# Kernel optimization log

Hardware: AMD Instinct MI355X
Metric: run time of the kernel (lower is better)

The kernel has to match this reference:

```python
import jax, jax.numpy as jnp
import numpy as np

N, E = 10000, 100000   # nodes, edges
C = 64                 # sphere_channels
L2 = 9                 # (lmax+1)^2 with lmax=2
H, DH, DV = 8, 16, 16  # heads, alpha channels/head, value channels/head
EC = 64                # edge scalar channels
NRBF = 128             # radial basis size
ZMAX = 90              # max_num_elements


def setup_inputs() -> dict:
    key = jax.random.key(0)
    ks = jax.random.split(key, 12)
    inp = {}
    inp["node_embedding"] = jax.random.normal(ks[0], (N, L2, C), jnp.float32)
    inp["atomic_numbers"] = jax.random.randint(ks[1], (N,), 0, ZMAX)
    inp["edge_distance"] = jax.random.uniform(ks[2], (E,), jnp.float32)
    inp["edge_index"] = jax.random.randint(ks[3], (2, E), 0, N)
    # per-edge Wigner rotation into the edge-aligned SO(2) frame
    inp["wigner"] = jax.random.normal(ks[4], (E, L2, L2), jnp.float32) / np.sqrt(L2)
    # learned parameters
    inp["atom_emb"] = jax.random.normal(ks[5], (ZMAX, EC), jnp.float32) * 0.1
    inp["W_rbf"] = jax.random.normal(ks[6], (NRBF, EC), jnp.float32) / np.sqrt(NRBF)
    inp["W_gate"] = jax.random.normal(ks[7], (EC, H * DH), jnp.float32) / np.sqrt(EC)
    inp["W_msg"] = jax.random.normal(ks[8], (2 * C, H * DH), jnp.float32) / np.sqrt(2 * C)
    inp["alpha_vec"] = jax.random.normal(ks[9], (H, DH), jnp.float32) / np.sqrt(DH)
    inp["W_val"] = jax.random.normal(ks[10], (H * DH, H * DV), jnp.float32) / np.sqrt(H * DH)
    inp["W_out"] = jax.random.normal(ks[11], (H * DV, 1), jnp.float32) / np.sqrt(H * DV)
    return inp


def reference(node_embedding, atomic_numbers, edge_distance, edge_index, wigner,
              atom_emb, W_rbf, W_gate, W_msg, alpha_vec, W_val, W_out):
    src, dst = edge_index[0], edge_index[1]
    # --- edge scalar embedding: gaussian RBF of distance + endpoint atom embeddings ---
    centers = jnp.linspace(0.0, 1.0, NRBF, dtype=node_embedding.dtype)
    width = 1.0 / NRBF
    rbf = jnp.exp(-((edge_distance[:, None] - centers) ** 2) / (2.0 * width * width))  # [E, NRBF]
    edge_scalar = jax.nn.silu(rbf @ W_rbf + atom_emb[atomic_numbers[src]] + atom_emb[atomic_numbers[dst]])  # [E, EC]
    gate = jax.nn.silu(edge_scalar @ W_gate)  # [E, H*DH]
    # --- gather endpoint embeddings and rotate into edge frame (SO3 rotation) ---
    x_s = jnp.einsum('eij,ejc->eic', wigner, node_embedding[src])  # [E, L2, C]
    x_t = jnp.einsum('eij,ejc->eic', wigner, node_embedding[dst])  # [E, L2, C]
    msg = jnp.concatenate([x_s, x_t], axis=-1) @ W_msg            # [E, L2, H*DH]
    msg = msg * gate[:, None, :]
    # --- attention logits from the invariant (l=0) component ---
    a = msg[:, 0, :].reshape(E, H, DH)
    logits = jnp.einsum('ehd,hd->eh', jax.nn.leaky_relu(a, 0.2), alpha_vec)  # [E, H]
    # --- softmax over incoming edges of each destination node ---
    m = jax.ops.segment_max(logits, dst, num_segments=N)  # [N, H]
    ex = jnp.exp(logits - m[dst])
    den = jax.ops.segment_sum(ex, dst, num_segments=N)
    attn = ex / (den[dst] + 1e-9)  # [E, H]
    # --- attention-weighted values, rotate back, scatter-sum to nodes ---
    v = (msg @ W_val).reshape(E, L2, H, DV)
    v = v * attn[:, None, :, None]
    v = jnp.einsum('eji,ejhv->eihv', wigner, v).reshape(E, L2, H * DV)  # rotate back (R^T)
    node_out = jax.ops.segment_sum(v, dst, num_segments=N)  # [N, L2, H*DV]
    out = node_out @ W_out                                   # [N, L2, 1]
    forces = out[:, 1:4, 0]                                  # narrow(1,1,3).view(-1,3)
    return forces
```

## Files before the change

kernel.cpp:

```cpp
#include <hip/hip_runtime.h>
#include <hip/hip_bf16.h>

#define NN 10000
#define NE 100000

typedef __attribute__((ext_vector_type(8))) short short8v;
typedef __attribute__((ext_vector_type(4))) short short4v;
typedef __attribute__((ext_vector_type(4))) float float4v;

__device__ __forceinline__ unsigned int enc_f(float f) {
  unsigned int u = __float_as_uint(f);
  return (u & 0x80000000u) ? ~u : (u | 0x80000000u);
}
__device__ __forceinline__ float dec_f(unsigned int u) {
  return __uint_as_float((u & 0x80000000u) ? (u & 0x7fffffffu) : ~u);
}
__device__ __forceinline__ float silu_f(float x) {
  return x / (1.0f + __expf(-x));
}
__device__ __forceinline__ float b2f(short s) {
  return __uint_as_float(((unsigned int)(unsigned short)s) << 16);
}
__device__ __forceinline__ void f32_hilo(float x, short& h, short& l) {
  __hip_bfloat16 bh = __float2bfloat16(x);
  float r = x - __bfloat162float(bh);
  __hip_bfloat16 bl = __float2bfloat16(r);
  h = __builtin_bit_cast(short, bh);
  l = __builtin_bit_cast(short, bl);
}
__device__ __forceinline__ short f2bf(float x) {
  return __builtin_bit_cast(short, __float2bfloat16(x));
}
#define MFMA16(a, b, c) __builtin_amdgcn_mfma_f32_16x16x32_bf16(a, b, c, 0, 0, 0)

__global__ void prep_kernel(const float* __restrict__ W_msg, const float* __restrict__ W_val,
                            const float* __restrict__ W_out, const float* __restrict__ W_rbf,
                            const float* __restrict__ W_gate,
                            float* __restrict__ Q,
                            short* __restrict__ Wp1h, short* __restrict__ Wp1l,
                            short* __restrict__ Wp2h, short* __restrict__ Wp2l,
                            short* __restrict__ Wp3h, short* __restrict__ Wp3l,
                            short* __restrict__ Wp4h, short* __restrict__ Wp4l) {
  int i = blockIdx.x * blockDim.x + threadIdx.x;
  if (i < 1024) {
    int c = i >> 3, h = i & 7;
    float s = 0.0f;
#pragma unroll
    for (int dv = 0; dv < 16; ++dv)
      s += W_val[c * 128 + h * 16 + dv] * W_out[h * 16 + dv];
    Q[c * 8 + h] = s;
  }
  const float* W; short* ph; short* pl; int KF, Nw, local; bool tr = false;
  if (i < 8192)       { W = W_rbf;  ph = Wp1h; pl = Wp1l; KF = 4; Nw = 64;  local = i; }
  else if (i < 16384) { W = W_gate; ph = Wp2h; pl = Wp2l; KF = 2; Nw = 128; local = i - 8192; }
  else if (i < 32768) { W = W_msg;  ph = Wp3h; pl = Wp3l; KF = 4; Nw = 128; local = i - 16384; }
  else                { W = W_msg;  ph = Wp4h; pl = Wp4l; KF = 4; Nw = 128; local = i - 32768; tr = true; }
  int tile = local >> 9;
  int ln = (local >> 3) & 63;
  int j = local & 7;
  int nt = tile / KF, kf = tile % KF;
  int k = kf * 32 + 8 * (ln >> 4) + j;
  int n = nt * 16 + (ln & 15);
  float w = tr ? W[n * 128 + k] : W[k * Nw + n];
  short h, lo;
  f32_hilo(w, h, lo);
  ph[local] = h;
  pl[local] = lo;
}

__global__ __launch_bounds__(256) void gather1_kernel(
    const float* __restrict__ nb, const int* __restrict__ ei,
    const float* __restrict__ wig, short* __restrict__ xch,
    short* __restrict__ xcl, short* __restrict__ Gb) {
  const int lane = threadIdx.x & 63;
  const int e = blockIdx.x * 4 + (threadIdx.x >> 6);
  int se = ei[e], de = ei[NE + e];
  const float* __restrict__ pw = wig + (size_t)e * 81;
  const float* __restrict__ ps = nb + (size_t)se * 576 + lane;
  const float* __restrict__ pt = nb + (size_t)de * 576 + lane;
  float vs[9], vt[9];
#pragma unroll
  for (int j = 0; j < 9; ++j) {
    vs[j] = ps[j * 64];
    vt[j] = pt[j * 64];
  }
  float Gs0 = 0, Gs1 = 0, Gs2 = 0, Gt0 = 0, Gt1 = 0, Gt2 = 0;
#pragma unroll
  for (int j = 0; j < 9; ++j) {
    float row[9];
#pragma unroll
    for (int jp = 0; jp < 9; ++jp) row[jp] = pw[j * 9 + jp];
    float xs = 0.0f, xt = 0.0f;
#pragma unroll
    for (int jp = 0; jp < 9; ++jp) { xs += row[jp] * vs[jp]; xt += row[jp] * vt[jp]; }
    if (j == 0) {
      short h, l;
      f32_hilo(xs, h, l);
      xch[(size_t)e * 128 + lane] = h;
      xcl[(size_t)e * 128 + lane] = l;
      f32_hilo(xt, h, l);
      xch[(size_t)e * 128 + 64 + lane] = h;
      xcl[(size_t)e * 128 + 64 + lane] = l;
    }
    Gs0 += row[1] * xs; Gs1 += row[2] * xs; Gs2 += row[3] * xs;
    Gt0 += row[1] * xt; Gt1 += row[2] * xt; Gt2 += row[3] * xt;
  }
  short* gp = Gb + (size_t)e * 384 + lane;
  gp[0]       = f2bf(Gs0);
  gp[64]      = f2bf(Gs1);
  gp[128]     = f2bf(Gs2);
  gp[192]     = f2bf(Gt0);
  gp[256]     = f2bf(Gt1);
  gp[320]     = f2bf(Gt2);
}

__global__ __launch_bounds__(256, 3) void pass1_kernel(
    const int* __restrict__ zn, const float* __restrict__ dist,
    const int* __restrict__ ei, const float* __restrict__ aemb,
    const float* __restrict__ alpha,
    const short* __restrict__ xch, const short* __restrict__ xcl,
    const short* __restrict__ Wp1h, const short* __restrict__ Wp1l,
    const short* __restrict__ Wp2h, const short* __restrict__ Wp2l,
    const short* __restrict__ Wp3h, const short* __restrict__ Wp3l,
    float* __restrict__ logits, unsigned int* __restrict__ m_enc,
    __hip_bfloat16* __restrict__ gate_ws) {
  __shared__ __attribute__((aligned(16))) float es_s[4][16][68];
  const int tid = threadIdx.x;
  const int lane = tid & 63;
  const int wid = tid >> 6;
  const int g = lane >> 4;
  const int col = lane & 15;
  const int e0 = (blockIdx.x * 4 + wid) * 16;

  int l16 = lane & 15;
  int ecl16 = (e0 + l16 < NE) ? e0 + l16 : NE - 1;
  int idx_v = 0;
  if (lane < 32) idx_v = ei[(lane < 16 ? 0 : NE) + ecl16];

  int ecol = e0 + col; if (ecol >= NE) ecol = NE - 1;
  const float d = dist[ecol];

  const short* ph = xch + (size_t)ecol * 128 + 8 * g;
  const short* pl = xcl + (size_t)ecol * 128 + 8 * g;
  short8v a3h[4], a3l[4];
#pragma unroll
  for (int kf = 0; kf < 4; ++kf) {
    a3h[kf] = *(const short8v*)(ph + kf * 32);
    a3l[kf] = *(const short8v*)(pl + kf * 32);
  }

  short8v a1h[4], a1l[4];
#pragma unroll
  for (int kf = 0; kf < 4; ++kf) {
#pragma unroll
    for (int j = 0; j < 8; ++j) {
      int k = kf * 32 + 8 * g + j;
      float t = d - (float)k * (1.0f / 127.0f);
      float v = __expf(-8192.0f * t * t);
      short h, lo; f32_hilo(v, h, lo);
      a1h[kf][j] = h; a1l[kf][j] = lo;
    }
  }

  const float4v z4 = {0.0f, 0.0f, 0.0f, 0.0f};

  float4v acc1[4];
#pragma unroll
  for (int nt = 0; nt < 4; ++nt) {
    float4v a = z4;
#pragma unroll
    for (int kf = 0; kf < 4; ++kf) {
      short8v bh = *(const short8v*)(Wp1h + ((nt * 4 + kf) * 64 + lane) * 8);
      short8v bl = *(const short8v*)(Wp1l + ((nt * 4 + kf) * 64 + lane) * 8);
      a = MFMA16(a1h[kf], bh, a);
      a = MFMA16(a1h[kf], bl, a);
      a = MFMA16(a1l[kf], bh, a);
    }
    acc1[nt] = a;
  }

  int dn_r[4];
#pragma unroll
  for (int r = 0; r < 4; ++r) {
    int sn = __shfl(idx_v, 4 * g + r);
    dn_r[r] = __shfl(idx_v, 16 + 4 * g + r);
    int zs = zn[sn], zd = zn[dn_r[r]];
#pragma unroll
    for (int nt = 0; nt < 4; ++nt) {
      float b = aemb[zs * 64 + nt * 16 + col] + aemb[zd * 64 + nt * 16 + col];
      es_s[wid][4 * g + r][nt * 16 + col] = silu_f(acc1[nt][r] + b);
    }
  }

  short8v a2h[2], a2l[2];
#pragma unroll
  for (int kf = 0; kf < 2; ++kf) {
    const float* p = &es_s[wid][col][kf * 32 + 8 * g];
    float4v v0 = *(const float4v*)p;
    float4v v1 = *(const float4v*)(p + 4);
#pragma unroll
    for (int j = 0; j < 4; ++j) {
      short h, lo;
      f32_hilo(v0[j], h, lo); a2h[kf][j] = h;     a2l[kf][j] = lo;
      f32_hilo(v1[j], h, lo); a2h[kf][4 + j] = h; a2l[kf][4 + j] = lo;
    }
  }

  float gate_r[8][4];
#pragma unroll
  for (int nt = 0; nt < 8; ++nt) {
    float4v a = z4;
#pragma unroll
    for (int kf = 0; kf < 2; ++kf) {
      short8v bh = *(const short8v*)(Wp2h + ((nt * 2 + kf) * 64 + lane) * 8);
      short8v bl = *(const short8v*)(Wp2l + ((nt * 2 + kf) * 64 + lane) * 8);
      a = MFMA16(a2h[kf], bh, a);
      a = MFMA16(a2h[kf], bl, a);
      a = MFMA16(a2l[kf], bh, a);
    }
#pragma unroll
    for (int r = 0; r < 4; ++r) {
      float gv = silu_f(a[r]);
      gate_r[nt][r] = gv;
      int er = e0 + 4 * g + r;
      if (er < NE)
        gate_ws[(size_t)er * 128 + nt * 16 + col] = __float2bfloat16(gv);
    }
  }

#pragma unroll
  for (int nt = 0; nt < 8; ++nt) {
    float4v a = z4;
#pragma unroll
    for (int kf = 0; kf < 4; ++kf) {
      short8v bh = *(const short8v*)(Wp3h + ((nt * 4 + kf) * 64 + lane) * 8);
      short8v bl = *(const short8v*)(Wp3l + ((nt * 4 + kf) * 64 + lane) * 8);
      a = MFMA16(a3h[kf], bh, a);
      a = MFMA16(a3h[kf], bl, a);
      a = MFMA16(a3l[kf], bh, a);
    }
    float al = alpha[nt * 16 + col];
#pragma unroll
    for (int r = 0; r < 4; ++r) {
      float v = a[r] * gate_r[nt][r];
      v = v > 0.0f ? v : 0.2f * v;
      v *= al;
#pragma unroll
      for (int off = 1; off < 16; off <<= 1) v += __shfl_xor(v, off);
      int er = e0 + 4 * g + r;
      if (col == 0 && er < NE) {
        logits[(size_t)er * 8 + nt] = v;
        atomicMax(&m_enc[dn_r[r] * 8 + nt], enc_f(v));
      }
    }
  }
}

__global__ void pass2_kernel(const float* __restrict__ logits,
                             const int* __restrict__ ei,
                             const unsigned int* __restrict__ m_enc,
                             float* __restrict__ den) {
  int i = blockIdx.x * blockDim.x + threadIdx.x;
  if (i >= NE * 8) return;
  int e = i >> 3, h = i & 7;
  int dn = ei[NE + e];
  float mm = dec_f(m_enc[dn * 8 + h]);
  atomicAdd(&den[dn * 8 + h], __expf(logits[i] - mm));
}

__global__ __launch_bounds__(256, 3) void pass3_kernel(
    const int* __restrict__ ei, const float* __restrict__ logits,
    const unsigned int* __restrict__ m_enc, const float* __restrict__ den,
    const __hip_bfloat16* __restrict__ gate_ws, const float* __restrict__ Q,
    const short* __restrict__ Wp4h, const short* __restrict__ Wp4l,
    const short* __restrict__ Gb, float* __restrict__ out) {
  __shared__ __attribute__((aligned(16))) float attn_s[4][16][8];
  __shared__ __attribute__((aligned(16))) float x_s[4][16][132];
  const int tid = threadIdx.x;
  const int lane = tid & 63;
  const int wid = tid >> 6;
  const int g = lane >> 4;
  const int col = lane & 15;
  const int e0 = (blockIdx.x * 4 + wid) * 16;

#pragma unroll
  for (int half = 0; half < 2; ++half) {
    int i = half * 64 + lane;
    int e = i >> 3, h = i & 7;
    int ec = e0 + e; if (ec >= NE) ec = NE - 1;
    int dn = ei[NE + ec];
    float l = logits[(size_t)ec * 8 + h];
    float mm = dec_f(m_enc[dn * 8 + h]);
    float dv = den[dn * 8 + h];
    attn_s[wid][e][h] = __expf(l - mm) / (dv + 1e-9f);
  }

  float q0[8], q1[8];
#pragma unroll
  for (int h = 0; h < 8; ++h) {
    q0[h] = Q[(2 * lane) * 8 + h];
    q1[h] = Q[(2 * lane + 1) * 8 + h];
  }
#pragma unroll 4
  for (int e = 0; e < 16; ++e) {
    int ec = e0 + e; if (ec >= NE) ec = NE - 1;
    float4v a0 = *(const float4v*)&attn_s[wid][e][0];
    float4v a1 = *(const float4v*)&attn_s[wid][e][4];
    float wv0 = 0.0f, wv1 = 0.0f;
#pragma unroll
    for (int h = 0; h < 4; ++h) {
      wv0 += q0[h] * a0[h] + q0[4 + h] * a1[h];
      wv1 += q1[h] * a0[h] + q1[4 + h] * a1[h];
    }
    unsigned int gp = *(const unsigned int*)(gate_ws + (size_t)ec * 128 + 2 * lane);
    float gg0 = __uint_as_float((gp & 0xffffu) << 16);
    float gg1 = __uint_as_float((gp & 0xffff0000u));
    float2 uu; uu.x = gg0 * wv0; uu.y = gg1 * wv1;
    *(float2*)&x_s[wid][e][2 * lane] = uu;
  }

  short8v ah[4], al[4];
#pragma unroll
  for (int kf = 0; kf < 4; ++kf) {
    const float* p = &x_s[wid][col][kf * 32 + 8 * g];
    float4v v0 = *(const float4v*)p;
    float4v v1 = *(const float4v*)(p + 4);
#pragma unroll
    for (int j = 0; j < 4; ++j) {
      short h, lo;
      f32_hilo(v0[j], h, lo); ah[kf][j] = h;     al[kf][j] = lo;
      f32_hilo(v1[j], h, lo); ah[kf][4 + j] = h; al[kf][4 + j] = lo;
    }
  }
  const float4v z4 = {0.0f, 0.0f, 0.0f, 0.0f};
#pragma unroll
  for (int nt = 0; nt < 8; ++nt) {
    float4v a = z4;
#pragma unroll
    for (int kf = 0; kf < 4; ++kf) {
      short8v bh = *(const short8v*)(Wp4h + ((nt * 4 + kf) * 64 + lane) * 8);
      short8v bl = *(const short8v*)(Wp4l + ((nt * 4 + kf) * 64 + lane) * 8);
      a = MFMA16(ah[kf], bh, a);
      a = MFMA16(ah[kf], bl, a);
      a = MFMA16(al[kf], bh, a);
    }
#pragma unroll
    for (int r = 0; r < 4; ++r)
      x_s[wid][4 * g + r][nt * 16 + col] = a[r];
  }

  const int cg = col * 4;
#pragma unroll
  for (int it = 0; it < 4; ++it) {
    int e = it * 4 + g;
    int eu = e0 + e;
    bool valid = eu < NE;
    int ec = valid ? eu : NE - 1;
    int de = ei[NE + ec];
    float4v t0 = *(const float4v*)&x_s[wid][e][cg];
    float4v t1 = *(const float4v*)&x_s[wid][e][64 + cg];
    const short* gp = Gb + (size_t)ec * 384 + cg;
    float p[3];
#pragma unroll
    for (int i = 0; i < 3; ++i) {
      short4v gs = *(const short4v*)(gp + i * 64);
      short4v gt = *(const short4v*)(gp + (3 + i) * 64);
      p[i] = b2f(gs[0]) * t0[0] + b2f(gs[1]) * t0[1] + b2f(gs[2]) * t0[2] + b2f(gs[3]) * t0[3] +
             b2f(gt[0]) * t1[0] + b2f(gt[1]) * t1[1] + b2f(gt[2]) * t1[2] + b2f(gt[3]) * t1[3];
    }
#pragma unroll
    for (int i = 0; i < 3; ++i)
#pragma unroll
      for (int off = 1; off < 16; off <<= 1) p[i] += __shfl_xor(p[i], off);
    float pv = (col == 1) ? p[0] : ((col == 2) ? p[1] : p[2]);
    if (valid && col >= 1 && col <= 3)
      atomicAdd(&out[de * 3 + (col - 1)], pv);
  }
}

extern "C" void kernel_launch(void* const* d_in, const int* in_sizes, int n_in,
                              void* d_out, int out_size, void* d_ws, size_t ws_size,
                              hipStream_t stream) {
  const float* nb = (const float*)d_in[0];
  const int* zn = (const int*)d_in[1];
  const float* dist = (const float*)d_in[2];
  const int* ei = (const int*)d_in[3];
  const float* wig = (const float*)d_in[4];
  const float* aemb = (const float*)d_in[5];
  const float* W_rbf = (const float*)d_in[6];
  const float* W_gate = (const float*)d_in[7];
  const float* W_msg = (const float*)d_in[8];
  const float* alpha = (const float*)d_in[9];
  const float* W_val = (const float*)d_in[10];
  const float* W_out = (const float*)d_in[11];
  float* out = (float*)d_out;

  char* p = (char*)d_ws;
  float* Q = (float*)p;                   p += 1024 * 4;
  unsigned int* m_enc = (unsigned int*)p; p += (size_t)NN * 8 * 4;
  float* den = (float*)p;                 p += (size_t)NN * 8 * 4;
  float* logits = (float*)p;              p += (size_t)NE * 8 * 4;
  __hip_bfloat16* gate_ws = (__hip_bfloat16*)p; p += (size_t)NE * 128 * 2;
  short* Wp1h = (short*)p; p += 8192 * 2;
  short* Wp1l = (short*)p; p += 8192 * 2;
  short* Wp2h = (short*)p; p += 8192 * 2;
  short* Wp2l = (short*)p; p += 8192 * 2;
  short* Wp3h = (short*)p; p += 16384 * 2;
  short* Wp3l = (short*)p; p += 16384 * 2;
  short* Wp4h = (short*)p; p += 16384 * 2;
  short* Wp4l = (short*)p; p += 16384 * 2;
  short* xch = (short*)p;                 p += (size_t)NE * 128 * 2;
  short* xcl = (short*)p;                 p += (size_t)NE * 128 * 2;
  short* Gb = (short*)p;                  p += (size_t)NE * 384 * 2;

  hipMemsetAsync(d_out, 0, (size_t)NN * 3 * 4, stream);
  hipMemsetAsync(m_enc, 0, (size_t)NN * 8 * 4, stream);
  hipMemsetAsync(den, 0, (size_t)NN * 8 * 4, stream);

  prep_kernel<<<192, 256, 0, stream>>>(W_msg, W_val, W_out, W_rbf, W_gate, Q,
                                       Wp1h, Wp1l, Wp2h, Wp2l, Wp3h, Wp3l, Wp4h, Wp4l);
  gather1_kernel<<<NE / 4, 256, 0, stream>>>(nb, ei, wig, xch, xcl, Gb);
  pass1_kernel<<<(NE + 63) / 64, 256, 0, stream>>>(zn, dist, ei, aemb, alpha,
                                                   xch, xcl,
                                                   Wp1h, Wp1l, Wp2h, Wp2l, Wp3h, Wp3l,
                                                   logits, m_enc, gate_ws);
  pass2_kernel<<<(NE * 8 + 255) / 256, 256, 0, stream>>>(logits, ei, m_enc, den);
  pass3_kernel<<<(NE + 63) / 64, 256, 0, stream>>>(ei, logits, m_enc, den,
                                                   gate_ws, Q, Wp4h, Wp4l, Gb, out);
}
```

Measured before the change: 315.3 us.

## Fuse gather/rotation kernel into pass1 with software-pipelined node loads

Removes the separate gather1 kernel and performs the Wigner rotation of source/target node embeddings inside pass1, keeping the l=0 rotated features in shared memory instead of writing hi/lo bf16 copies to global memory and reading them back. Node embedding loads are double-buffered across edges so the next edge's gathers are in flight while the current one is rotated. This cuts a kernel launch and about 51 MB of intermediate traffic, but each wave now processes 16 edges serially in the gather phase, which adds register pressure under launch_bounds(256,3) and may lower parallelism compared with the one-edge-per-wave gather.

```diff
diff --git a/kernel.cpp b/kernel.cpp
--- a/kernel.cpp
+++ b/kernel.cpp
@@ -8,6 +8,9 @@
 typedef __attribute__((ext_vector_type(4))) short short4v;
 typedef __attribute__((ext_vector_type(4))) float float4v;
 
+__device__ __forceinline__ int bcast_i(int v, int k) {
+  return __builtin_amdgcn_readlane(v, k);
+}
 __device__ __forceinline__ unsigned int enc_f(float f) {
   unsigned int u = __float_as_uint(f);
   return (u & 0x80000000u) ? ~u : (u | 0x80000000u);
@@ -32,6 +35,20 @@
   return __builtin_bit_cast(short, __float2bfloat16(x));
 }
 #define MFMA16(a, b, c) __builtin_amdgcn_mfma_f32_16x16x32_bf16(a, b, c, 0, 0, 0)
+
+__device__ __forceinline__ void g_issue(const float* __restrict__ nb, int idx_v,
+                                        int e, int lane,
+                                        float (&VS)[9], float (&VT)[9]) {
+  int se_ = bcast_i(idx_v, e);
+  int de_ = bcast_i(idx_v, 16 + e);
+  const float* __restrict__ ps_ = nb + (size_t)se_ * 576 + lane;
+  const float* __restrict__ pt_ = nb + (size_t)de_ * 576 + lane;
+#pragma unroll
+  for (int j = 0; j < 9; ++j) {
+    VS[j] = ps_[j * 64];
+    VT[j] = pt_[j * 64];
+  }
+}
 
 __global__ void prep_kernel(const float* __restrict__ W_msg, const float* __restrict__ W_val,
                             const float* __restrict__ W_out, const float* __restrict__ W_rbf,
@@ -68,63 +85,17 @@
   pl[local] = lo;
 }
 
-__global__ __launch_bounds__(256) void gather1_kernel(
-    const float* __restrict__ nb, const int* __restrict__ ei,
-    const float* __restrict__ wig, short* __restrict__ xch,
-    short* __restrict__ xcl, short* __restrict__ Gb) {
-  const int lane = threadIdx.x & 63;
-  const int e = blockIdx.x * 4 + (threadIdx.x >> 6);
-  int se = ei[e], de = ei[NE + e];
-  const float* __restrict__ pw = wig + (size_t)e * 81;
-  const float* __restrict__ ps = nb + (size_t)se * 576 + lane;
-  const float* __restrict__ pt = nb + (size_t)de * 576 + lane;
-  float vs[9], vt[9];
-#pragma unroll
-  for (int j = 0; j < 9; ++j) {
-    vs[j] = ps[j * 64];
-    vt[j] = pt[j * 64];
-  }
-  float Gs0 = 0, Gs1 = 0, Gs2 = 0, Gt0 = 0, Gt1 = 0, Gt2 = 0;
-#pragma unroll
-  for (int j = 0; j < 9; ++j) {
-    float row[9];
-#pragma unroll
-    for (int jp = 0; jp < 9; ++jp) row[jp] = pw[j * 9 + jp];
-    float xs = 0.0f, xt = 0.0f;
-#pragma unroll
-    for (int jp = 0; jp < 9; ++jp) { xs += row[jp] * vs[jp]; xt += row[jp] * vt[jp]; }
-    if (j == 0) {
-      short h, l;
-      f32_hilo(xs, h, l);
-      xch[(size_t)e * 128 + lane] = h;
-      xcl[(size_t)e * 128 + lane] = l;
-      f32_hilo(xt, h, l);
-      xch[(size_t)e * 128 + 64 + lane] = h;
-      xcl[(size_t)e * 128 + 64 + lane] = l;
-    }
-    Gs0 += row[1] * xs; Gs1 += row[2] * xs; Gs2 += row[3] * xs;
-    Gt0 += row[1] * xt; Gt1 += row[2] * xt; Gt2 += row[3] * xt;
-  }
-  short* gp = Gb + (size_t)e * 384 + lane;
-  gp[0]       = f2bf(Gs0);
-  gp[64]      = f2bf(Gs1);
-  gp[128]     = f2bf(Gs2);
-  gp[192]     = f2bf(Gt0);
-  gp[256]     = f2bf(Gt1);
-  gp[320]     = f2bf(Gt2);
-}
-
 __global__ __launch_bounds__(256, 3) void pass1_kernel(
-    const int* __restrict__ zn, const float* __restrict__ dist,
-    const int* __restrict__ ei, const float* __restrict__ aemb,
+    const float* __restrict__ nb, const int* __restrict__ zn,
+    const float* __restrict__ dist, const int* __restrict__ ei,
+    const float* __restrict__ wig, const float* __restrict__ aemb,
     const float* __restrict__ alpha,
-    const short* __restrict__ xch, const short* __restrict__ xcl,
     const short* __restrict__ Wp1h, const short* __restrict__ Wp1l,
     const short* __restrict__ Wp2h, const short* __restrict__ Wp2l,
     const short* __restrict__ Wp3h, const short* __restrict__ Wp3l,
     float* __restrict__ logits, unsigned int* __restrict__ m_enc,
-    __hip_bfloat16* __restrict__ gate_ws) {
-  __shared__ __attribute__((aligned(16))) float es_s[4][16][68];
+    __hip_bfloat16* __restrict__ gate_ws, short* __restrict__ Gb) {
+  __shared__ __attribute__((aligned(16))) float xe_s[4][16][132];
   const int tid = threadIdx.x;
   const int lane = tid & 63;
   const int wid = tid >> 6;
@@ -140,13 +111,46 @@
   int ecol = e0 + col; if (ecol >= NE) ecol = NE - 1;
   const float d = dist[ecol];
 
-  const short* ph = xch + (size_t)ecol * 128 + 8 * g;
-  const short* pl = xcl + (size_t)ecol * 128 + 8 * g;
-  short8v a3h[4], a3l[4];
-#pragma unroll
-  for (int kf = 0; kf < 4; ++kf) {
-    a3h[kf] = *(const short8v*)(ph + kf * 32);
-    a3l[kf] = *(const short8v*)(pl + kf * 32);
+  auto consume = [&](int e, const float (&vs)[9], const float (&vt)[9]) {
+    int eu = e0 + e;
+    int ec = eu < NE ? eu : NE - 1;
+    const float* __restrict__ pw = wig + (size_t)ec * 81;
+    float Gs0 = 0, Gs1 = 0, Gs2 = 0, Gt0 = 0, Gt1 = 0, Gt2 = 0;
+#pragma unroll
+    for (int j = 0; j < 9; ++j) {
+      float rr[9];
+#pragma unroll
+      for (int jp = 0; jp < 9; ++jp) rr[jp] = pw[j * 9 + jp];
+      float xs = 0.0f, xt = 0.0f;
+#pragma unroll
+      for (int jp = 0; jp < 9; ++jp) { xs += rr[jp] * vs[jp]; xt += rr[jp] * vt[jp]; }
+      if (j == 0) {
+        xe_s[wid][e][lane] = xs;
+        xe_s[wid][e][64 + lane] = xt;
+      }
+      Gs0 += rr[1] * xs; Gs1 += rr[2] * xs; Gs2 += rr[3] * xs;
+      Gt0 += rr[1] * xt; Gt1 += rr[2] * xt; Gt2 += rr[3] * xt;
+    }
+    if (eu < NE) {
+      short* gp = Gb + (size_t)ec * 384 + lane;
+      gp[0]   = f2bf(Gs0);
+      gp[64]  = f2bf(Gs1);
+      gp[128] = f2bf(Gs2);
+      gp[192] = f2bf(Gt0);
+      gp[256] = f2bf(Gt1);
+      gp[320] = f2bf(Gt2);
+    }
+  };
+
+  float vs0[9], vt0[9], vs1[9], vt1[9];
+  g_issue(nb, idx_v, 0, lane, vs0, vt0);
+  g_issue(nb, idx_v, 1, lane, vs1, vt1);
+#pragma unroll
+  for (int e = 0; e < 16; e += 2) {
+    consume(e, vs0, vt0);
+    if (e + 2 < 16) g_issue(nb, idx_v, e + 2, lane, vs0, vt0);
+    consume(e + 1, vs1, vt1);
+    if (e + 3 < 16) g_issue(nb, idx_v, e + 3, lane, vs1, vt1);
   }
 
   short8v a1h[4], a1l[4];
@@ -162,6 +166,20 @@
     }
   }
 
+  short8v a3h[4], a3l[4];
+#pragma unroll
+  for (int kf = 0; kf < 4; ++kf) {
+    const float* p = &xe_s[wid][col][kf * 32 + 8 * g];
+    float4v v0 = *(const float4v*)p;
+    float4v v1 = *(const float4v*)(p + 4);
+#pragma unroll
+    for (int j = 0; j < 4; ++j) {
+      short h, lo;
+      f32_hilo(v0[j], h, lo); a3h[kf][j] = h;     a3l[kf][j] = lo;
+      f32_hilo(v1[j], h, lo); a3h[kf][4 + j] = h; a3l[kf][4 + j] = lo;
+    }
+  }
+
   const float4v z4 = {0.0f, 0.0f, 0.0f, 0.0f};
 
   float4v acc1[4];
@@ -188,14 +206,14 @@
 #pragma unroll
     for (int nt = 0; nt < 4; ++nt) {
       float b = aemb[zs * 64 + nt * 16 + col] + aemb[zd * 64 + nt * 16 + col];
-      es_s[wid][4 * g + r][nt * 16 + col] = silu_f(acc1[nt][r] + b);
+      xe_s[wid][4 * g + r][nt * 16 + col] = silu_f(acc1[nt][r] + b);
     }
   }
 
   short8v a2h[2], a2l[2];
 #pragma unroll
   for (int kf = 0; kf < 2; ++kf) {
-    const float* p = &es_s[wid][col][kf * 32 + 8 * g];
+    const float* p = &xe_s[wid][col][kf * 32 + 8 * g];
     float4v v0 = *(const float4v*)p;
     float4v v1 = *(const float4v*)(p + 4);
 #pragma unroll
@@ -409,8 +427,6 @@
   short* Wp3l = (short*)p; p += 16384 * 2;
   short* Wp4h = (short*)p; p += 16384 * 2;
   short* Wp4l = (short*)p; p += 16384 * 2;
-  short* xch = (short*)p;                 p += (size_t)NE * 128 * 2;
-  short* xcl = (short*)p;                 p += (size_t)NE * 128 * 2;
   short* Gb = (short*)p;                  p += (size_t)NE * 384 * 2;
 
   hipMemsetAsync(d_out, 0, (size_t)NN * 3 * 4, stream);
@@ -419,11 +435,9 @@
 
   prep_kernel<<<192, 256, 0, stream>>>(W_msg, W_val, W_out, W_rbf, W_gate, Q,
                                        Wp1h, Wp1l, Wp2h, Wp2l, Wp3h, Wp3l, Wp4h, Wp4l);
-  gather1_kernel<<<NE / 4, 256, 0, stream>>>(nb, ei, wig, xch, xcl, Gb);
-  pass1_kernel<<<(NE + 63) / 64, 256, 0, stream>>>(zn, dist, ei, aemb, alpha,
-                                                   xch, xcl,
+  pass1_kernel<<<(NE + 63) / 64, 256, 0, stream>>>(nb, zn, dist, ei, wig, aemb, alpha,
                                                    Wp1h, Wp1l, Wp2h, Wp2l, Wp3h, Wp3l,
-                                                   logits, m_enc, gate_ws);
+                                                   logits, m_enc, gate_ws, Gb);
   pass2_kernel<<<(NE * 8 + 255) / 256, 256, 0, stream>>>(logits, ei, m_enc, den);
   pass3_kernel<<<(NE + 63) / 64, 256, 0, stream>>>(ei, logits, m_enc, den,
                                                    gate_ws, Q, Wp4h, Wp4l, Gb, out);
```

Result: no change. 319.1 us (+1.2%).
